# Kernel optimization log

Measured on AMD Instinct MI355X. Metric: run time of the kernel, lower is better.

The kernel has to match this reference:

```python
import jax, jax.numpy as jnp
import numpy as np

EMBED_DIM = 256
NUM_HEADS = 8
HEAD_DIM = EMBED_DIM // NUM_HEADS
FFN_DIM = 4 * EMBED_DIM
B, N = 2, 2048


def _layernorm(x, w, b, eps=1e-5):
    mu = jnp.mean(x, axis=-1, keepdims=True)
    var = jnp.var(x, axis=-1, keepdims=True)
    return (x - mu) * jax.lax.rsqrt(var + eps) * w + b


def setup_inputs() -> dict:
    key = jax.random.key(0)
    ks = jax.random.split(key, 16)
    s = 0.02
    d = {
        "x": jax.random.normal(ks[0], (B, N, EMBED_DIM), jnp.float32),
        "influence_matrix": jax.random.uniform(ks[1], (B, N, N), jnp.float32),
        "qw": jax.random.normal(ks[2], (EMBED_DIM, EMBED_DIM), jnp.float32) * s,
        "qb": jnp.zeros((EMBED_DIM,), jnp.float32),
        "kw": jax.random.normal(ks[3], (EMBED_DIM, EMBED_DIM), jnp.float32) * s,
        "kb": jnp.zeros((EMBED_DIM,), jnp.float32),
        "vw": jax.random.normal(ks[4], (EMBED_DIM, EMBED_DIM), jnp.float32) * s,
        "vb": jnp.zeros((EMBED_DIM,), jnp.float32),
        "ow": jax.random.normal(ks[5], (EMBED_DIM, EMBED_DIM), jnp.float32) * s,
        "ob": jnp.zeros((EMBED_DIM,), jnp.float32),
        "w1": jax.random.normal(ks[6], (EMBED_DIM, FFN_DIM), jnp.float32) * s,
        "b1": jnp.zeros((FFN_DIM,), jnp.float32),
        "w2": jax.random.normal(ks[7], (FFN_DIM, EMBED_DIM), jnp.float32) * s,
        "b2": jnp.zeros((EMBED_DIM,), jnp.float32),
        "ln1_w": jnp.ones((EMBED_DIM,), jnp.float32),
        "ln1_b": jnp.zeros((EMBED_DIM,), jnp.float32),
        "ln2_w": jnp.ones((EMBED_DIM,), jnp.float32),
        "ln2_b": jnp.zeros((EMBED_DIM,), jnp.float32),
    }
    return d


def reference(x, influence_matrix, qw, qb, kw, kb, vw, vb, ow, ob,
              w1, b1, w2, b2, ln1_w, ln1_b, ln2_w, ln2_b):
    # --- pre-norm attention with multiplicative influence bias ---
    h = _layernorm(x, ln1_w, ln1_b)
    q = (h @ qw + qb).reshape(B, N, NUM_HEADS, HEAD_DIM)
    k = (h @ kw + kb).reshape(B, N, NUM_HEADS, HEAD_DIM)
    v = (h @ vw + vb).reshape(B, N, NUM_HEADS, HEAD_DIM)
    scores = jnp.einsum('bnhd,bmhd->bhnm', q, k) / np.sqrt(HEAD_DIM).astype(np.float32)
    scores = scores * (1.0 + influence_matrix[:, None, :, :])  # multiplicative bias
    attn = jax.nn.softmax(scores, axis=-1)
    out = jnp.einsum('bhnm,bmhd->bnhd', attn, v).reshape(B, N, EMBED_DIM)
    x = x + out @ ow + ob
    # --- GELU FFN (torch GELU is exact erf form) ---
    h2 = _layernorm(x, ln2_w, ln2_b)
    ff = jax.nn.gelu(h2 @ w1 + b1, approximate=False) @ w2 + b2
    return x + ff
```

## Files before the change

kernel.cpp:

```cpp
#include <hip/hip_runtime.h>
#include <hip/hip_bf16.h>
#include <math.h>

#define NSEQ 2048
#define DMODEL 256

typedef __attribute__((ext_vector_type(8))) __bf16 bf16x8;
typedef __attribute__((ext_vector_type(4))) float f32x4;
typedef __attribute__((ext_vector_type(8))) unsigned short ushort8;
typedef __attribute__((ext_vector_type(4))) unsigned short ushort4e;
typedef __attribute__((ext_vector_type(4))) unsigned int uint4e;

__device__ __forceinline__ unsigned short f2b(float f) {
    return __builtin_bit_cast(unsigned short, (__bf16)f);
}
__device__ __forceinline__ float b2f(unsigned short u) {
    return (float)__builtin_bit_cast(__bf16, u);
}
__device__ __forceinline__ bf16x8 ldfrag16(const void* p) {
    return __builtin_bit_cast(bf16x8, *(const uint4e*)p);
}

__global__ __launch_bounds__(256)
void ln_kernel(const float* __restrict__ x, const float* __restrict__ g,
               const float* __restrict__ b, __bf16* __restrict__ out)
{
    const int row  = blockIdx.x * 4 + (threadIdx.x >> 6);
    const int lane = threadIdx.x & 63;
    const float4 v = *(const float4*)(x + (size_t)row * DMODEL + lane * 4);
    float s  = v.x + v.y + v.z + v.w;
    float s2 = v.x*v.x + v.y*v.y + v.z*v.z + v.w*v.w;
#pragma unroll
    for (int off = 32; off; off >>= 1) {
        s  += __shfl_xor(s, off);
        s2 += __shfl_xor(s2, off);
    }
    const float mu = s * (1.0f / DMODEL);
    const float rs = rsqrtf(s2 * (1.0f / DMODEL) - mu * mu + 1e-5f);
    const float4 gv = *(const float4*)(g + lane * 4);
    const float4 bv = *(const float4*)(b + lane * 4);
    __bf16* o = out + (size_t)row * DMODEL + lane * 4;
    o[0] = (__bf16)((v.x - mu) * rs * gv.x + bv.x);
    o[1] = (__bf16)((v.y - mu) * rs * gv.y + bv.y);
    o[2] = (__bf16)((v.z - mu) * rs * gv.z + bv.z);
    o[3] = (__bf16)((v.w - mu) * rs * gv.w + bv.w);
}

__device__ __forceinline__ void gemm_core(
    const __bf16* __restrict__ A, const float* __restrict__ W,
    const float* __restrict__ bias, const float* __restrict__ resid,
    void* __restrict__ outp, int M, int N, int K, int epi, short* Bs)
{
    const int t    = threadIdx.x;
    const int lane = t & 63;
    const int w    = t >> 6;
    const int wr   = w & 1, wc = w >> 1;
    const int g    = lane >> 4, c = lane & 15;
    const int row0 = blockIdx.y * 32;
    const int col0 = blockIdx.x * 64;

    f32x4 acc[2] = {};
    const int bj = t & 63, bk = (t >> 6) * 8;

    for (int ks = 0; ks < K; ks += 256) {
        if (ks) __syncthreads();
#pragma unroll
        for (int kt = 0; kt < 256; kt += 32) {
            const float* wp = W + (size_t)(ks + kt + bk) * N + col0 + bj;
            const float f0 = wp[0];               const float f1 = wp[(size_t)N];
            const float f2 = wp[(size_t)2 * N];   const float f3 = wp[(size_t)3 * N];
            const float f4 = wp[(size_t)4 * N];   const float f5 = wp[(size_t)5 * N];
            const float f6 = wp[(size_t)6 * N];   const float f7 = wp[(size_t)7 * N];
            uint4e uu;
            uu.x = (unsigned)f2b(f0) | ((unsigned)f2b(f1) << 16);
            uu.y = (unsigned)f2b(f2) | ((unsigned)f2b(f3) << 16);
            uu.z = (unsigned)f2b(f4) | ((unsigned)f2b(f5) << 16);
            uu.w = (unsigned)f2b(f6) | ((unsigned)f2b(f7) << 16);
            *(uint4e*)(Bs + bj * 264 + kt + bk) = uu;
        }
        __syncthreads();
        const __bf16* arow = A + (size_t)(row0 + wr * 16 + c) * K + ks + g * 8;
        const short* b0p = Bs + (wc * 32 + c) * 264 + g * 8;
        const short* b1p = b0p + 16 * 264;
#pragma unroll
        for (int kc = 0; kc < 256; kc += 32) {
            const bf16x8 a  = ldfrag16(arow + kc);
            const bf16x8 b0 = ldfrag16(b0p + kc);
            const bf16x8 b1 = ldfrag16(b1p + kc);
            acc[0] = __builtin_amdgcn_mfma_f32_16x16x32_bf16(a, b0, acc[0], 0, 0, 0);
            acc[1] = __builtin_amdgcn_mfma_f32_16x16x32_bf16(a, b1, acc[1], 0, 0, 0);
        }
    }

    if (epi == 3) {
        __syncthreads();
#pragma unroll
        for (int ch = 0; ch < 2; ++ch)
#pragma unroll
        for (int r = 0; r < 4; ++r) {
            const int cl = wc * 32 + ch * 16 + c;
            Bs[(wr * 16 + g * 4 + r) * 66 + cl] = (short)f2b(acc[ch][r] + bias[col0 + cl]);
        }
        __syncthreads();
        const int d = t >> 2, mc = (t & 3) * 8;
        ushort8 o0;
#pragma unroll
        for (int j = 0; j < 8; ++j)
            o0[j] = (unsigned short)Bs[(mc + j) * 66 + d];
        __bf16* vt = (__bf16*)outp;
        *(uint4e*)(vt + (size_t)(col0 + d) * M + row0 + mc) = __builtin_bit_cast(uint4e, o0);
    } else {
#pragma unroll
        for (int ch = 0; ch < 2; ++ch)
#pragma unroll
        for (int r = 0; r < 4; ++r) {
            const int row = row0 + wr * 16 + g * 4 + r;
            const int col = col0 + wc * 32 + ch * 16 + c;
            float val = acc[ch][r] + bias[col];
            if (epi == 0) {
                ((__bf16*)outp)[(size_t)row * N + col] = (__bf16)val;
            } else if (epi == 1) {
                val = 0.5f * val * (1.0f + erff(val * 0.70710678118654752f));
                ((__bf16*)outp)[(size_t)row * N + col] = (__bf16)val;
            } else {
                ((float*)outp)[(size_t)row * N + col] = resid[(size_t)row * N + col] + val;
            }
        }
    }
}

template<int EPI>
__global__ __launch_bounds__(256, 4)
void gemm_kernel(const __bf16* __restrict__ A, const float* __restrict__ W,
                 const float* __restrict__ bias, const float* __restrict__ resid,
                 void* __restrict__ outp, int M, int N, int K)
{
    __shared__ short Bs[64 * 264];
    gemm_core(A, W, bias, resid, outp, M, N, K, EPI, Bs);
}

__global__ __launch_bounds__(256, 4)
void qkv_kernel(const __bf16* __restrict__ A,
                const float* __restrict__ qw, const float* __restrict__ qb,
                const float* __restrict__ kw, const float* __restrict__ kb,
                const float* __restrict__ vw, const float* __restrict__ vb,
                __bf16* __restrict__ qo, __bf16* __restrict__ ko,
                __bf16* __restrict__ vto)
{
    __shared__ short Bs[64 * 264];
    const int z = blockIdx.z;
    const float* W    = (z == 0) ? qw : (z == 1) ? kw : vw;
    const float* bias = (z == 0) ? qb : (z == 1) ? kb : vb;
    void* outp        = (z == 0) ? (void*)qo : (z == 1) ? (void*)ko : (void*)vto;
    gemm_core(A, W, bias, nullptr, outp, 4096, 256, 256, (z == 2) ? 3 : 0, Bs);
}

__global__ __launch_bounds__(512, 4)
void attn_kernel(const __bf16* __restrict__ Q, const __bf16* __restrict__ K,
                 const __bf16* __restrict__ VT, const float* __restrict__ infl,
                 __bf16* __restrict__ Opart, float* __restrict__ ml)
{
    __shared__ short Pm[8][16][72];

    const int t    = threadIdx.x;
    const int lane = t & 63;
    const int w    = t >> 6;
    const int g    = lane >> 4, c = lane & 15;
    const int b    = blockIdx.z;
    const int sp   = blockIdx.y;
    const int n0   = blockIdx.x * 16;
    const int m_start = sp * 1024;

    const bf16x8 qf = ldfrag16(Q + (size_t)(b * NSEQ + n0 + c) * DMODEL + w * 32 + g * 8);

    const __bf16* Khead = K  + (size_t)(b * NSEQ + c) * DMODEL + w * 32 + g * 8;
    const __bf16* Vhead = VT + (size_t)(w * 32 + c) * (2 * NSEQ) + b * NSEQ + g * 8;
    const float*  irow  = infl + (size_t)(b * NSEQ + n0 + c) * NSEQ + g * 4;

    f32x4 Oacc[2] = {};
    float lsum = 0.0f;
    const float scale = 0.17677669529663687f;

    bf16x8 kf[4];
    float4 finf[4];
#pragma unroll
    for (int mt = 0; mt < 4; ++mt) {
        kf[mt]   = ldfrag16(Khead + (size_t)(m_start + mt * 16) * DMODEL);
        finf[mt] = *(const float4*)(irow + m_start + mt * 16);
    }

    for (int it = 0; it < 16; ++it) {
        const int m0 = m_start + (it << 6);
        const int mn = m_start + (((it + 1) & 15) << 6);

        f32x4 s[4];
#pragma unroll
        for (int mt = 0; mt < 4; ++mt) {
            f32x4 z4 = {0.f, 0.f, 0.f, 0.f};
            s[mt] = __builtin_amdgcn_mfma_f32_16x16x32_bf16(kf[mt], qf, z4, 0, 0, 0);
        }
#pragma unroll
        for (int mt = 0; mt < 4; ++mt)
            kf[mt] = ldfrag16(Khead + (size_t)(mn + mt * 16) * DMODEL);
        bf16x8 vfa[4];
#pragma unroll
        for (int ks = 0; ks < 2; ++ks)
#pragma unroll
            for (int dt = 0; dt < 2; ++dt)
                vfa[ks * 2 + dt] =
                    ldfrag16(Vhead + (size_t)(dt * 16) * (2 * NSEQ) + m0 + ks * 32);

        float p[4][4];
#pragma unroll
        for (int mt = 0; mt < 4; ++mt)
#pragma unroll
            for (int r = 0; r < 4; ++r) {
                const float t1 = s[mt][r] * scale;
                const float pe = __expf(t1 + t1 * finf[mt][r]);
                p[mt][r] = pe;
                lsum += pe;
            }
#pragma unroll
        for (int mt = 0; mt < 4; ++mt)
            finf[mt] = *(const float4*)(irow + mn + mt * 16);

#pragma unroll
        for (int mt = 0; mt < 4; ++mt) {
            ushort4e pk;
            pk.x = f2b(p[mt][0]); pk.y = f2b(p[mt][1]);
            pk.z = f2b(p[mt][2]); pk.w = f2b(p[mt][3]);
            *(ushort4e*)&Pm[w][c][mt * 16 + g * 4] = pk;
        }
        asm volatile("" ::: "memory");

#pragma unroll
        for (int ks = 0; ks < 2; ++ks) {
            const bf16x8 pf = ldfrag16(&Pm[w][c][ks * 32 + g * 8]);
            Oacc[0] = __builtin_amdgcn_mfma_f32_16x16x32_bf16(pf, vfa[ks * 2 + 0], Oacc[0], 0, 0, 0);
            Oacc[1] = __builtin_amdgcn_mfma_f32_16x16x32_bf16(pf, vfa[ks * 2 + 1], Oacc[1], 0, 0, 0);
        }
    }

    lsum += __shfl_xor(lsum, 16);
    lsum += __shfl_xor(lsum, 32);
    if (lane < 16)
        ml[((size_t)(sp * 4096 + b * NSEQ + n0 + lane)) * 8 + w] = lsum;

#pragma unroll
    for (int r = 0; r < 4; ++r) {
        const int grow = b * NSEQ + n0 + g * 4 + r;
#pragma unroll
        for (int dt = 0; dt < 2; ++dt)
            Opart[(size_t)(sp * 4096 + grow) * 256 + w * 32 + dt * 16 + c] =
                (__bf16)Oacc[dt][r];
    }
}

__global__ __launch_bounds__(256)
void combine_kernel(const __bf16* __restrict__ Opart, const float* __restrict__ ml,
                    __bf16* __restrict__ ao)
{
    const int tid = blockIdx.x * 256 + threadIdx.x;
    const int row = tid >> 5;
    const int d0  = (tid & 31) * 8;
    const int h   = d0 >> 5;
    const float l0 = ml[(size_t)row * 8 + h];
    const float l1 = ml[(size_t)(4096 + row) * 8 + h];
    const float inv = 1.0f / (l0 + l1);
    const ushort8 xa = *(const ushort8*)(Opart + (size_t)row * 256 + d0);
    const ushort8 xb = *(const ushort8*)(Opart + (size_t)(4096 + row) * 256 + d0);
    __bf16 o[8];
#pragma unroll
    for (int e = 0; e < 8; ++e)
        o[e] = (__bf16)((b2f(xa[e]) + b2f(xb[e])) * inv);
    *(uint4e*)(ao + (size_t)row * 256 + d0) = *(uint4e*)o;
}

extern "C" void kernel_launch(void* const* d_in, const int* in_sizes, int n_in,
                              void* d_out, int out_size, void* d_ws, size_t ws_size,
                              hipStream_t stream)
{
    (void)in_sizes; (void)n_in; (void)out_size; (void)ws_size;
    const float* x    = (const float*)d_in[0];
    const float* infl = (const float*)d_in[1];
    const float* qw   = (const float*)d_in[2];
    const float* qb   = (const float*)d_in[3];
    const float* kw   = (const float*)d_in[4];
    const float* kb   = (const float*)d_in[5];
    const float* vw   = (const float*)d_in[6];
    const float* vb   = (const float*)d_in[7];
    const float* ow   = (const float*)d_in[8];
    const float* ob_  = (const float*)d_in[9];
    const float* w1   = (const float*)d_in[10];
    const float* b1   = (const float*)d_in[11];
    const float* w2   = (const float*)d_in[12];
    const float* b2   = (const float*)d_in[13];
    const float* ln1w = (const float*)d_in[14];
    const float* ln1b = (const float*)d_in[15];
    const float* ln2w = (const float*)d_in[16];
    const float* ln2b = (const float*)d_in[17];
    float* out = (float*)d_out;

    char* ws = (char*)d_ws;
    __bf16* h     = (__bf16*)(ws +  0 * 1048576ull);
    __bf16* q     = (__bf16*)(ws +  2 * 1048576ull);
    __bf16* kx    = (__bf16*)(ws +  4 * 1048576ull);
    __bf16* vt    = (__bf16*)(ws +  6 * 1048576ull);
    __bf16* Opart = (__bf16*)(ws +  8 * 1048576ull);
    float*  mlbuf = (float*) (ws + 12 * 1048576ull);
    __bf16* ao    = (__bf16*)(ws + 13 * 1048576ull);
    float*  x2    = (float*) (ws + 15 * 1048576ull);
    __bf16* h2    = (__bf16*)(ws + 19 * 1048576ull);
    __bf16* ff    = (__bf16*)(ws + 21 * 1048576ull);

    ln_kernel<<<1024, 256, 0, stream>>>(x, ln1w, ln1b, h);
    qkv_kernel<<<dim3(4, 128, 3), 256, 0, stream>>>(h, qw, qb, kw, kb, vw, vb, q, kx, vt);
    attn_kernel<<<dim3(128, 2, 2), 512, 0, stream>>>(q, kx, vt, infl, Opart, mlbuf);
    combine_kernel<<<512, 256, 0, stream>>>(Opart, mlbuf, ao);
    gemm_kernel<2><<<dim3(4, 128),  256, 0, stream>>>(ao, ow, ob_, x,      x2,  4096,  256,  256);
    ln_kernel<<<1024, 256, 0, stream>>>(x2, ln2w, ln2b, h2);
    gemm_kernel<1><<<dim3(16, 128), 256, 0, stream>>>(h2, w1, b1, nullptr, ff,  4096, 1024,  256);
    gemm_kernel<2><<<dim3(4, 128),  256, 0, stream>>>(ff, w2, b2, x2,     out, 4096,  256, 1024);
}
```

Baseline: 250.0 us.

## Pre-transpose weights to bf16, drop LDS staging in GEMMs, restage influence via LDS

Adds transpose kernels that convert every fp32 weight matrix to a transposed bf16 copy once per call. The GEMMs then read B fragments directly from global memory with no LDS staging or per-block fp32-to-bf16 conversion, using a new tile shape. The attention kernel is also reworked: influence rows are staged cooperatively through a double-buffered LDS tile with coalesced loads, the score MFMA operands are swapped, and K loads are prefetched into separate registers. This trades three extra small kernel launches for cheaper GEMM inner loops and better influence-matrix coalescing.

```diff
diff --git a/kernel.cpp b/kernel.cpp
--- a/kernel.cpp
+++ b/kernel.cpp
@@ -8,7 +8,6 @@
 typedef __attribute__((ext_vector_type(8))) __bf16 bf16x8;
 typedef __attribute__((ext_vector_type(4))) float f32x4;
 typedef __attribute__((ext_vector_type(8))) unsigned short ushort8;
-typedef __attribute__((ext_vector_type(4))) unsigned short ushort4e;
 typedef __attribute__((ext_vector_type(4))) unsigned int uint4e;
 
 __device__ __forceinline__ unsigned short f2b(float f) {
@@ -19,6 +18,42 @@
 }
 __device__ __forceinline__ bf16x8 ldfrag16(const void* p) {
     return __builtin_bit_cast(bf16x8, *(const uint4e*)p);
+}
+
+__global__ __launch_bounds__(256)
+void tr_kernel(const float* __restrict__ in, __bf16* __restrict__ out, int K, int N)
+{
+    __shared__ float tile[32][33];
+    const int tx = threadIdx.x & 31, ty = threadIdx.x >> 5;
+    const int n0 = blockIdx.x * 32, k0 = blockIdx.y * 32;
+#pragma unroll
+    for (int j = 0; j < 4; ++j)
+        tile[ty * 4 + j][tx] = in[(size_t)(k0 + ty * 4 + j) * N + n0 + tx];
+    __syncthreads();
+#pragma unroll
+    for (int j = 0; j < 4; ++j)
+        out[(size_t)(n0 + ty * 4 + j) * K + k0 + tx] = (__bf16)tile[tx][ty * 4 + j];
+}
+
+__global__ __launch_bounds__(256)
+void tr4_kernel(const float* __restrict__ w0, const float* __restrict__ w1,
+                const float* __restrict__ w2, const float* __restrict__ w3,
+                __bf16* __restrict__ o0, __bf16* __restrict__ o1,
+                __bf16* __restrict__ o2, __bf16* __restrict__ o3)
+{
+    __shared__ float tile[32][33];
+    const int z = blockIdx.z;
+    const float* in = (z == 0) ? w0 : (z == 1) ? w1 : (z == 2) ? w2 : w3;
+    __bf16* out     = (z == 0) ? o0 : (z == 1) ? o1 : (z == 2) ? o2 : o3;
+    const int tx = threadIdx.x & 31, ty = threadIdx.x >> 5;
+    const int n0 = blockIdx.x * 32, k0 = blockIdx.y * 32;
+#pragma unroll
+    for (int j = 0; j < 4; ++j)
+        tile[ty * 4 + j][tx] = in[(size_t)(k0 + ty * 4 + j) * 256 + n0 + tx];
+    __syncthreads();
+#pragma unroll
+    for (int j = 0; j < 4; ++j)
+        out[(size_t)(n0 + ty * 4 + j) * 256 + k0 + tx] = (__bf16)tile[tx][ty * 4 + j];
 }
 
 __global__ __launch_bounds__(256)
@@ -46,77 +81,49 @@
     o[3] = (__bf16)((v.w - mu) * rs * gv.w + bv.w);
 }
 
-__device__ __forceinline__ void gemm_core(
-    const __bf16* __restrict__ A, const float* __restrict__ W,
+template<int WN>
+__device__ __forceinline__ void gemm2_core(
+    const __bf16* __restrict__ A, const __bf16* __restrict__ WT,
     const float* __restrict__ bias, const float* __restrict__ resid,
-    void* __restrict__ outp, int M, int N, int K, int epi, short* Bs)
-{
-    const int t    = threadIdx.x;
-    const int lane = t & 63;
-    const int w    = t >> 6;
-    const int wr   = w & 1, wc = w >> 1;
-    const int g    = lane >> 4, c = lane & 15;
-    const int row0 = blockIdx.y * 32;
-    const int col0 = blockIdx.x * 64;
-
-    f32x4 acc[2] = {};
-    const int bj = t & 63, bk = (t >> 6) * 8;
-
-    for (int ks = 0; ks < K; ks += 256) {
-        if (ks) __syncthreads();
-#pragma unroll
-        for (int kt = 0; kt < 256; kt += 32) {
-            const float* wp = W + (size_t)(ks + kt + bk) * N + col0 + bj;
-            const float f0 = wp[0];               const float f1 = wp[(size_t)N];
-            const float f2 = wp[(size_t)2 * N];   const float f3 = wp[(size_t)3 * N];
-            const float f4 = wp[(size_t)4 * N];   const float f5 = wp[(size_t)5 * N];
-            const float f6 = wp[(size_t)6 * N];   const float f7 = wp[(size_t)7 * N];
-            uint4e uu;
-            uu.x = (unsigned)f2b(f0) | ((unsigned)f2b(f1) << 16);
-            uu.y = (unsigned)f2b(f2) | ((unsigned)f2b(f3) << 16);
-            uu.z = (unsigned)f2b(f4) | ((unsigned)f2b(f5) << 16);
-            uu.w = (unsigned)f2b(f6) | ((unsigned)f2b(f7) << 16);
-            *(uint4e*)(Bs + bj * 264 + kt + bk) = uu;
+    void* __restrict__ outp, int M, int N, int K, int epi, short* LDSv)
+{
+    const int t = threadIdx.x, lane = t & 63, w = t >> 6;
+    const int g = lane >> 4, c = lane & 15;
+    const int row0 = blockIdx.y * 64, col0 = blockIdx.x * WN;
+
+    const __bf16* arow = A  + (size_t)(row0 + w * 16 + c) * K + g * 8;
+    const __bf16* brow = WT + (size_t)(col0 + c) * K + g * 8;
+
+    f32x4 acc[WN / 16] = {};
+#pragma unroll 8
+    for (int k = 0; k < K; k += 32) {
+        const bf16x8 a = ldfrag16(arow + k);
+#pragma unroll
+        for (int dt = 0; dt < WN / 16; ++dt) {
+            const bf16x8 bb = ldfrag16(brow + (size_t)dt * 16 * K + k);
+            acc[dt] = __builtin_amdgcn_mfma_f32_16x16x32_bf16(a, bb, acc[dt], 0, 0, 0);
         }
+    }
+
+    if (epi == 3) {
+#pragma unroll
+        for (int dt = 0; dt < WN / 16; ++dt)
+#pragma unroll
+        for (int r = 0; r < 4; ++r)
+            LDSv[(dt * 16 + c) * 72 + w * 16 + g * 4 + r] =
+                (short)f2b(acc[dt][r] + bias[col0 + dt * 16 + c]);
         __syncthreads();
-        const __bf16* arow = A + (size_t)(row0 + wr * 16 + c) * K + ks + g * 8;
-        const short* b0p = Bs + (wc * 32 + c) * 264 + g * 8;
-        const short* b1p = b0p + 16 * 264;
-#pragma unroll
-        for (int kc = 0; kc < 256; kc += 32) {
-            const bf16x8 a  = ldfrag16(arow + kc);
-            const bf16x8 b0 = ldfrag16(b0p + kc);
-            const bf16x8 b1 = ldfrag16(b1p + kc);
-            acc[0] = __builtin_amdgcn_mfma_f32_16x16x32_bf16(a, b0, acc[0], 0, 0, 0);
-            acc[1] = __builtin_amdgcn_mfma_f32_16x16x32_bf16(a, b1, acc[1], 0, 0, 0);
-        }
-    }
-
-    if (epi == 3) {
-        __syncthreads();
-#pragma unroll
-        for (int ch = 0; ch < 2; ++ch)
+        const int col = t >> 3, seg = t & 7;
+        const uint4e o = *(const uint4e*)&LDSv[col * 72 + seg * 8];
+        *(uint4e*)((__bf16*)outp + (size_t)(col0 + col) * M + row0 + seg * 8) = o;
+    } else {
+#pragma unroll
+        for (int dt = 0; dt < WN / 16; ++dt)
 #pragma unroll
         for (int r = 0; r < 4; ++r) {
-            const int cl = wc * 32 + ch * 16 + c;
-            Bs[(wr * 16 + g * 4 + r) * 66 + cl] = (short)f2b(acc[ch][r] + bias[col0 + cl]);
-        }
-        __syncthreads();
-        const int d = t >> 2, mc = (t & 3) * 8;
-        ushort8 o0;
-#pragma unroll
-        for (int j = 0; j < 8; ++j)
-            o0[j] = (unsigned short)Bs[(mc + j) * 66 + d];
-        __bf16* vt = (__bf16*)outp;
-        *(uint4e*)(vt + (size_t)(col0 + d) * M + row0 + mc) = __builtin_bit_cast(uint4e, o0);
-    } else {
-#pragma unroll
-        for (int ch = 0; ch < 2; ++ch)
-#pragma unroll
-        for (int r = 0; r < 4; ++r) {
-            const int row = row0 + wr * 16 + g * 4 + r;
-            const int col = col0 + wc * 32 + ch * 16 + c;
-            float val = acc[ch][r] + bias[col];
+            const int row = row0 + w * 16 + g * 4 + r;
+            const int col = col0 + dt * 16 + c;
+            float val = acc[dt][r] + bias[col];
             if (epi == 0) {
                 ((__bf16*)outp)[(size_t)row * N + col] = (__bf16)val;
             } else if (epi == 1) {
@@ -129,30 +136,31 @@
     }
 }
 
-template<int EPI>
-__global__ __launch_bounds__(256, 4)
-void gemm_kernel(const __bf16* __restrict__ A, const float* __restrict__ W,
+template<int WN, int EPI>
+__global__ __launch_bounds__(256)
+void gemm_kernel(const __bf16* __restrict__ A, const __bf16* __restrict__ WT,
                  const float* __restrict__ bias, const float* __restrict__ resid,
                  void* __restrict__ outp, int M, int N, int K)
 {
-    __shared__ short Bs[64 * 264];
-    gemm_core(A, W, bias, resid, outp, M, N, K, EPI, Bs);
-}
-
-__global__ __launch_bounds__(256, 4)
+    __shared__ short LDSv[32 * 72];
+    gemm2_core<WN>(A, WT, bias, resid, outp, M, N, K, EPI, LDSv);
+}
+
+__global__ __launch_bounds__(256)
 void qkv_kernel(const __bf16* __restrict__ A,
-                const float* __restrict__ qw, const float* __restrict__ qb,
-                const float* __restrict__ kw, const float* __restrict__ kb,
-                const float* __restrict__ vw, const float* __restrict__ vb,
+                const __bf16* __restrict__ qwT, const __bf16* __restrict__ kwT,
+                const __bf16* __restrict__ vwT,
+                const float* __restrict__ qb, const float* __restrict__ kb,
+                const float* __restrict__ vb,
                 __bf16* __restrict__ qo, __bf16* __restrict__ ko,
                 __bf16* __restrict__ vto)
 {
-    __shared__ short Bs[64 * 264];
+    __shared__ short LDSv[32 * 72];
     const int z = blockIdx.z;
-    const float* W    = (z == 0) ? qw : (z == 1) ? kw : vw;
-    const float* bias = (z == 0) ? qb : (z == 1) ? kb : vb;
-    void* outp        = (z == 0) ? (void*)qo : (z == 1) ? (void*)ko : (void*)vto;
-    gemm_core(A, W, bias, nullptr, outp, 4096, 256, 256, (z == 2) ? 3 : 0, Bs);
+    const __bf16* W    = (z == 0) ? qwT : (z == 1) ? kwT : vwT;
+    const float*  bias = (z == 0) ? qb  : (z == 1) ? kb  : vb;
+    void* outp         = (z == 0) ? (void*)qo : (z == 1) ? (void*)ko : (void*)vto;
+    gemm2_core<32>(A, W, bias, nullptr, outp, 4096, 256, 256, (z == 2) ? 3 : 0, LDSv);
 }
 
 __global__ __launch_bounds__(512, 4)
@@ -160,6 +168,7 @@
                  const __bf16* __restrict__ VT, const float* __restrict__ infl,
                  __bf16* __restrict__ Opart, float* __restrict__ ml)
 {
+    __shared__ float ilds[2][16][66];
     __shared__ short Pm[8][16][72];
 
     const int t    = threadIdx.x;
@@ -170,81 +179,95 @@
     const int sp   = blockIdx.y;
     const int n0   = blockIdx.x * 16;
     const int m_start = sp * 1024;
+    const float scale = 0.17677669529663687f;
 
     const bf16x8 qf = ldfrag16(Q + (size_t)(b * NSEQ + n0 + c) * DMODEL + w * 32 + g * 8);
 
     const __bf16* Khead = K  + (size_t)(b * NSEQ + c) * DMODEL + w * 32 + g * 8;
     const __bf16* Vhead = VT + (size_t)(w * 32 + c) * (2 * NSEQ) + b * NSEQ + g * 8;
-    const float*  irow  = infl + (size_t)(b * NSEQ + n0 + c) * NSEQ + g * 4;
+
+    const int irN = t >> 5, icol = (t & 31) * 2;
+    const float* iptr = infl + (size_t)(b * NSEQ + n0 + irN) * NSEQ + icol;
 
     f32x4 Oacc[2] = {};
-    float lsum = 0.0f;
-    const float scale = 0.17677669529663687f;
-
+    float lsum[4] = {0.f, 0.f, 0.f, 0.f};
+
+    float2 ireg = *(const float2*)(iptr + m_start);
     bf16x8 kf[4];
-    float4 finf[4];
-#pragma unroll
-    for (int mt = 0; mt < 4; ++mt) {
-        kf[mt]   = ldfrag16(Khead + (size_t)(m_start + mt * 16) * DMODEL);
-        finf[mt] = *(const float4*)(irow + m_start + mt * 16);
-    }
-
+#pragma unroll
+    for (int dt = 0; dt < 4; ++dt)
+        kf[dt] = ldfrag16(Khead + (size_t)(m_start + dt * 16) * DMODEL);
+
+    int buf = 0;
     for (int it = 0; it < 16; ++it) {
         const int m0 = m_start + (it << 6);
         const int mn = m_start + (((it + 1) & 15) << 6);
 
+        *(float2*)&ilds[buf][irN][icol] = ireg;
+        asm volatile("s_waitcnt lgkmcnt(0)" ::: "memory");
+        __builtin_amdgcn_s_barrier();
+
+        ireg = *(const float2*)(iptr + mn);
+        bf16x8 kn[4];
+#pragma unroll
+        for (int dt = 0; dt < 4; ++dt)
+            kn[dt] = ldfrag16(Khead + (size_t)(mn + dt * 16) * DMODEL);
+        bf16x8 vf[4];
+#pragma unroll
+        for (int ks = 0; ks < 2; ++ks)
+#pragma unroll
+            for (int dt = 0; dt < 2; ++dt)
+                vf[ks * 2 + dt] =
+                    ldfrag16(Vhead + (size_t)(dt * 16) * (2 * NSEQ) + m0 + ks * 32);
+
         f32x4 s[4];
 #pragma unroll
         for (int mt = 0; mt < 4; ++mt) {
             f32x4 z4 = {0.f, 0.f, 0.f, 0.f};
-            s[mt] = __builtin_amdgcn_mfma_f32_16x16x32_bf16(kf[mt], qf, z4, 0, 0, 0);
+            s[mt] = __builtin_amdgcn_mfma_f32_16x16x32_bf16(qf, kf[mt], z4, 0, 0, 0);
         }
+
+        float p[4][4];
 #pragma unroll
         for (int mt = 0; mt < 4; ++mt)
-            kf[mt] = ldfrag16(Khead + (size_t)(mn + mt * 16) * DMODEL);
-        bf16x8 vfa[4];
-#pragma unroll
-        for (int ks = 0; ks < 2; ++ks)
-#pragma unroll
-            for (int dt = 0; dt < 2; ++dt)
-                vfa[ks * 2 + dt] =
-                    ldfrag16(Vhead + (size_t)(dt * 16) * (2 * NSEQ) + m0 + ks * 32);
-
-        float p[4][4];
+#pragma unroll
+            for (int r = 0; r < 4; ++r) {
+                const float iw = scale + scale * ilds[buf][g * 4 + r][mt * 16 + c];
+                const float pe = __expf(s[mt][r] * iw);
+                p[mt][r] = pe;
+                lsum[r] += pe;
+            }
 #pragma unroll
         for (int mt = 0; mt < 4; ++mt)
 #pragma unroll
-            for (int r = 0; r < 4; ++r) {
-                const float t1 = s[mt][r] * scale;
-                const float pe = __expf(t1 + t1 * finf[mt][r]);
-                p[mt][r] = pe;
-                lsum += pe;
-            }
-#pragma unroll
-        for (int mt = 0; mt < 4; ++mt)
-            finf[mt] = *(const float4*)(irow + mn + mt * 16);
-
-#pragma unroll
-        for (int mt = 0; mt < 4; ++mt) {
-            ushort4e pk;
-            pk.x = f2b(p[mt][0]); pk.y = f2b(p[mt][1]);
-            pk.z = f2b(p[mt][2]); pk.w = f2b(p[mt][3]);
-            *(ushort4e*)&Pm[w][c][mt * 16 + g * 4] = pk;
-        }
+            for (int r = 0; r < 4; ++r)
+                Pm[w][g * 4 + r][mt * 16 + c] = (short)f2b(p[mt][r]);
         asm volatile("" ::: "memory");
 
 #pragma unroll
         for (int ks = 0; ks < 2; ++ks) {
             const bf16x8 pf = ldfrag16(&Pm[w][c][ks * 32 + g * 8]);
-            Oacc[0] = __builtin_amdgcn_mfma_f32_16x16x32_bf16(pf, vfa[ks * 2 + 0], Oacc[0], 0, 0, 0);
-            Oacc[1] = __builtin_amdgcn_mfma_f32_16x16x32_bf16(pf, vfa[ks * 2 + 1], Oacc[1], 0, 0, 0);
+            Oacc[0] = __builtin_amdgcn_mfma_f32_16x16x32_bf16(pf, vf[ks * 2 + 0], Oacc[0], 0, 0, 0);
+            Oacc[1] = __builtin_amdgcn_mfma_f32_16x16x32_bf16(pf, vf[ks * 2 + 1], Oacc[1], 0, 0, 0);
         }
-    }
-
-    lsum += __shfl_xor(lsum, 16);
-    lsum += __shfl_xor(lsum, 32);
-    if (lane < 16)
-        ml[((size_t)(sp * 4096 + b * NSEQ + n0 + lane)) * 8 + w] = lsum;
+
+#pragma unroll
+        for (int dt = 0; dt < 4; ++dt)
+            kf[dt] = kn[dt];
+        buf ^= 1;
+    }
+
+#pragma unroll
+    for (int off = 1; off < 16; off <<= 1)
+#pragma unroll
+        for (int r = 0; r < 4; ++r)
+            lsum[r] += __shfl_xor(lsum[r], off);
+
+    if (c == 0) {
+#pragma unroll
+        for (int r = 0; r < 4; ++r)
+            ml[((size_t)(sp * 4096 + b * NSEQ + n0 + g * 4 + r)) * 8 + w] = lsum[r];
+    }
 
 #pragma unroll
     for (int r = 0; r < 4; ++r) {
@@ -302,23 +325,33 @@
     float* out = (float*)d_out;
 
     char* ws = (char*)d_ws;
-    __bf16* h     = (__bf16*)(ws +  0 * 1048576ull);
-    __bf16* q     = (__bf16*)(ws +  2 * 1048576ull);
-    __bf16* kx    = (__bf16*)(ws +  4 * 1048576ull);
-    __bf16* vt    = (__bf16*)(ws +  6 * 1048576ull);
-    __bf16* Opart = (__bf16*)(ws +  8 * 1048576ull);
-    float*  mlbuf = (float*) (ws + 12 * 1048576ull);
-    __bf16* ao    = (__bf16*)(ws + 13 * 1048576ull);
-    float*  x2    = (float*) (ws + 15 * 1048576ull);
-    __bf16* h2    = (__bf16*)(ws + 19 * 1048576ull);
-    __bf16* ff    = (__bf16*)(ws + 21 * 1048576ull);
+    __bf16* qwT   = (__bf16*)(ws);
+    __bf16* kwT   = (__bf16*)(ws + (128u << 10));
+    __bf16* vwT   = (__bf16*)(ws + (256u << 10));
+    __bf16* owT   = (__bf16*)(ws + (384u << 10));
+    __bf16* w1T   = (__bf16*)(ws + (512u << 10));
+    __bf16* w2T   = (__bf16*)(ws + (1024u << 10));
+    __bf16* h     = (__bf16*)(ws +  2 * 1048576ull);
+    __bf16* q     = (__bf16*)(ws +  4 * 1048576ull);
+    __bf16* kx    = (__bf16*)(ws +  6 * 1048576ull);
+    __bf16* vt    = (__bf16*)(ws +  8 * 1048576ull);
+    __bf16* Opart = (__bf16*)(ws + 10 * 1048576ull);
+    float*  mlbuf = (float*) (ws + 14 * 1048576ull);
+    __bf16* ao    = (__bf16*)(ws + 15 * 1048576ull);
+    float*  x2    = (float*) (ws + 17 * 1048576ull);
+    __bf16* h2    = (__bf16*)(ws + 21 * 1048576ull);
+    __bf16* ff    = (__bf16*)(ws + 23 * 1048576ull);
+
+    tr4_kernel<<<dim3(8, 8, 4),  256, 0, stream>>>(qw, kw, vw, ow, qwT, kwT, vwT, owT);
+    tr_kernel <<<dim3(32, 8),    256, 0, stream>>>(w1, w1T, 256, 1024);
+    tr_kernel <<<dim3(8, 32),    256, 0, stream>>>(w2, w2T, 1024, 256);
 
     ln_kernel<<<1024, 256, 0, stream>>>(x, ln1w, ln1b, h);
-    qkv_kernel<<<dim3(4, 128, 3), 256, 0, stream>>>(h, qw, qb, kw, kb, vw, vb, q, kx, vt);
+    qkv_kernel<<<dim3(8, 64, 3), 256, 0, stream>>>(h, qwT, kwT, vwT, qb, kb, vb, q, kx, vt);
     attn_kernel<<<dim3(128, 2, 2), 512, 0, stream>>>(q, kx, vt, infl, Opart, mlbuf);
     combine_kernel<<<512, 256, 0, stream>>>(Opart, mlbuf, ao);
-    gemm_kernel<2><<<dim3(4, 128),  256, 0, stream>>>(ao, ow, ob_, x,      x2,  4096,  256,  256);
+    gemm_kernel<32, 2><<<dim3(8, 64),  256, 0, stream>>>(ao, owT, ob_, x,      x2,  4096,  256,  256);
     ln_kernel<<<1024, 256, 0, stream>>>(x2, ln2w, ln2b, h2);
-    gemm_kernel<1><<<dim3(16, 128), 256, 0, stream>>>(h2, w1, b1, nullptr, ff,  4096, 1024,  256);
-    gemm_kernel<2><<<dim3(4, 128),  256, 0, stream>>>(ff, w2, b2, x2,     out, 4096,  256, 1024);
-}
+    gemm_kernel<64, 1><<<dim3(16, 64), 256, 0, stream>>>(h2, w1T, b1, nullptr, ff,  4096, 1024,  256);
+    gemm_kernel<32, 2><<<dim3(8, 64),  256, 0, stream>>>(ff, w2T, b2, x2,     out, 4096,  256, 1024);
+}
```

New measurement: 255.5 us. 2.2% more time.
